# Optimization experiments

Hardware: AMD Instinct MI355X
Metric: run time of the kernel (lower is better)

Reference implementation:

```python
import jax, jax.numpy as jnp
import numpy as np

BS = 16   # block_size
SR = 16   # search_range


def setup_inputs() -> dict:
    key = jax.random.key(0)
    k1, k2 = jax.random.split(key)
    H, W = 2048, 2048
    current_frame = jax.random.uniform(k1, (H, W), dtype=jnp.float32)
    reference_frame = jax.random.uniform(k2, (H, W), dtype=jnp.float32)
    return {"current_frame": current_frame, "reference_frame": reference_frame}


def reference(current_frame, reference_frame):
    H, W = current_frame.shape
    bs, sr = BS, SR
    nby, nbx = H // bs, W // bs
    # zero-pad reference by search_range on all sides (matches F.pad constant 0)
    ref_p = jnp.pad(reference_frame, sr)
    # offsets in the same iteration order as the torch loops: dy outer, dx inner
    d = jnp.arange(-sr, sr + 1, dtype=jnp.int32)
    offs = jnp.stack(jnp.meshgrid(d, d, indexing="ij"), axis=-1).reshape(-1, 2)  # [(2sr+1)^2, 2]

    init = (
        jnp.full((nby, nbx), jnp.inf, dtype=jnp.float32),   # min_sad
        jnp.zeros((nby, nbx), dtype=jnp.float32),            # motion_x
        jnp.zeros((nby, nbx), dtype=jnp.float32),            # motion_y
    )

    def step(carry, off):
        best_sad, mx, my = carry
        dy, dx = off[0], off[1]
        # shifted reference plane: ref_padded[sr+dy : sr+dy+H, sr+dx : sr+dx+W]
        ref_shift = jax.lax.dynamic_slice(ref_p, (sr + dy, sr + dx), (H, W))
        # per-block SAD: sum |cur - ref| over each bs x bs tile
        sad = jnp.abs(current_frame - ref_shift).reshape(nby, bs, nbx, bs).sum(axis=(1, 3))
        better = sad < best_sad
        new_carry = (
            jnp.where(better, sad, best_sad),
            jnp.where(better, dx.astype(jnp.float32), mx),
            jnp.where(better, dy.astype(jnp.float32), my),
        )
        return new_carry, None

    (min_sad, motion_x, motion_y), _ = jax.lax.scan(step, init, offs)
    return motion_x, motion_y, min_sad
```

## Files before the change

### kernel.cpp

```cpp
#include <hip/hip_runtime.h>


#define HH 2048
#define WW 2048
#define NB 128
#define RSTR 100
#define CSTR 64
#define SCALE 16777216.0f
#define INV_SCALE 5.9604644775390625e-08f

__device__ __forceinline__ unsigned sadacc(unsigned a, unsigned b, unsigned c) {
    unsigned d;
    asm("v_sad_u32 %0, %1, %2, %3" : "=v"(d) : "v"(a), "v"(b), "v"(c));
    return d;
}

__launch_bounds__(256, 2)
__global__ void me_kernel(const float* __restrict__ cur,
                          const float* __restrict__ ref,
                          float* __restrict__ out) {
    __shared__ __align__(16) unsigned lds_ref[48 * RSTR];
    __shared__ __align__(16) unsigned lds_cur[16 * CSTR];

    const int tid = threadIdx.x;
    const int wg  = blockIdx.x;
    const int by  = wg >> 5;
    const int bx0 = (wg & 31) << 2;

    const int gy0 = by * 16 - 16;
    const int gx0 = bx0 * 16 - 16;
    for (int i = tid; i < 48 * 96; i += 256) {
        int r = i / 96;
        int c = i - r * 96;
        int gy = gy0 + r, gx = gx0 + c;
        float v = 0.f;
        if (gy >= 0 && gy < HH && gx >= 0 && gx < WW) v = ref[gy * WW + gx];
        lds_ref[r * RSTR + c] = (unsigned)(v * SCALE);
    }
    for (int i = tid; i < 16 * 64; i += 256) {
        int r = i >> 6, c = i & 63;
        lds_cur[i] = (unsigned)(cur[(by * 16 + r) * WW + bx0 * 16 + c] * SCALE);
    }
    __syncthreads();

    const int l  = tid & 63;
    const int b  = tid >> 6;
    const int n  = l >> 1;
    const int m  = l & 1;
    const int cb = b * 16;

    unsigned acc[16];
#pragma unroll
    for (int d = 0; d < 16; ++d) acc[d] = 0u;
    unsigned eA = 0u, eB = 0u;

    const unsigned* refbase = &lds_ref[n * RSTR + cb + 16 * m];
    const unsigned* curbase = &lds_cur[cb];
    const unsigned* eAbase  = &lds_ref[32 * RSTR + cb];
    const unsigned* eBbase  = &lds_ref[l * RSTR + cb + 32];

#pragma unroll 4
    for (int y = 0; y < 16; ++y) {
        unsigned cu[16];
#pragma unroll
        for (int q = 0; q < 4; ++q) {
            uint4 v = *(const uint4*)&curbase[y * CSTR + 4 * q];
            cu[4*q+0] = v.x; cu[4*q+1] = v.y; cu[4*q+2] = v.z; cu[4*q+3] = v.w;
        }
        unsigned rf[32];
#pragma unroll
        for (int q = 0; q < 8; ++q) {
            uint4 v = *(const uint4*)&refbase[y * RSTR + 4 * q];
            rf[4*q+0] = v.x; rf[4*q+1] = v.y; rf[4*q+2] = v.z; rf[4*q+3] = v.w;
        }
#pragma unroll
        for (int dd = 0; dd < 16; ++dd)
#pragma unroll
            for (int x = 0; x < 16; ++x)
                acc[dd] = sadacc(cu[x], rf[dd + x], acc[dd]);

        if (l < 33) {
#pragma unroll
            for (int x = 0; x < 16; ++x)
                eA = sadacc(cu[x], eAbase[y * RSTR + l + x], eA);
            unsigned eb[16];
#pragma unroll
            for (int q = 0; q < 4; ++q) {
                uint4 v = *(const uint4*)&eBbase[y * RSTR + 4 * q];
                eb[4*q+0] = v.x; eb[4*q+1] = v.y; eb[4*q+2] = v.z; eb[4*q+3] = v.w;
            }
#pragma unroll
            for (int x = 0; x < 16; ++x)
                eB = sadacc(cu[x], eb[x], eB);
        }
    }

    unsigned long long best = ~0ull;
#pragma unroll
    for (int dd = 0; dd < 16; ++dd) {
        unsigned long long p =
            ((unsigned long long)acc[dd] << 32) | (unsigned)(n * 33 + 16 * m + dd);
        best = p < best ? p : best;
    }
    if (l < 33) {
        unsigned long long pA =
            ((unsigned long long)eA << 32) | (unsigned)(32 * 33 + l);
        best = pA < best ? pA : best;
        unsigned long long pB =
            ((unsigned long long)eB << 32) | (unsigned)(l * 33 + 32);
        best = pB < best ? pB : best;
    }
#pragma unroll
    for (int s = 32; s > 0; s >>= 1) {
        unsigned long long o = __shfl_xor(best, s, 64);
        best = o < best ? o : best;
    }
    if (l == 0) {
        unsigned idx = (unsigned)(best & 0xffffffffu);
        unsigned sadu = (unsigned)(best >> 32);
        int dy = (int)(idx / 33) - 16;
        int dx = (int)(idx % 33) - 16;
        int bi = by * NB + (bx0 + b);
        out[bi]             = (float)dx;
        out[16384 + bi]     = (float)dy;
        out[2 * 16384 + bi] = (float)sadu * INV_SCALE;
    }
}

extern "C" void kernel_launch(void* const* d_in, const int* in_sizes, int n_in,
                              void* d_out, int out_size, void* d_ws, size_t ws_size,
                              hipStream_t stream) {
    const float* cur = (const float*)d_in[0];
    const float* ref = (const float*)d_in[1];
    float* out = (float*)d_out;
    (void)in_sizes; (void)n_in; (void)out_size; (void)d_ws; (void)ws_size;
    me_kernel<<<dim3(4096), dim3(256), 0, stream>>>(cur, ref, out);
}
```

Before: 219.4 us.

## Widen workgroup to eight blocks and rebalance edge-offset SAD work

Each workgroup now covers eight horizontally adjacent 16x16 blocks with 512 threads, sharing a 48x160 reference window. This cuts the halo loaded per block compared with four blocks per group. The two divergent edge-SAD paths, taken only by lanes below 33, become a single edge SAD per lane across all 64 lanes. The last corner offset is computed cooperatively with a wave reduction. The launch bounds change to (512, 8), which caps registers per thread and may cause spills given the 16 accumulators, 32 reference values and 16 current values held per thread.

Result: faster. 211.7 us (-3.5%).

```diff
diff --git a/kernel.cpp b/kernel.cpp
--- a/kernel.cpp
+++ b/kernel.cpp
@@ -4,18 +4,16 @@
 #define HH 2048
 #define WW 2048
 #define NB 128
-#define RSTR 100
-#define CSTR 64
+#define RSTR 164
+#define CSTR 128
 #define SCALE 16777216.0f
 #define INV_SCALE 5.9604644775390625e-08f
 
-__device__ __forceinline__ unsigned sadacc(unsigned a, unsigned b, unsigned c) {
-    unsigned d;
-    asm("v_sad_u32 %0, %1, %2, %3" : "=v"(d) : "v"(a), "v"(b), "v"(c));
-    return d;
+__device__ __forceinline__ void sadacc(unsigned a, unsigned b, unsigned& c) {
+    asm("v_sad_u32 %0, %1, %2, %0" : "+v"(c) : "v"(a), "v"(b));
 }
 
-__launch_bounds__(256, 2)
+__launch_bounds__(512, 8)
 __global__ void me_kernel(const float* __restrict__ cur,
                           const float* __restrict__ ref,
                           float* __restrict__ out) {
@@ -24,21 +22,25 @@
 
     const int tid = threadIdx.x;
     const int wg  = blockIdx.x;
-    const int by  = wg >> 5;
-    const int bx0 = (wg & 31) << 2;
+    const int by  = wg >> 4;
+    const int bx0 = (wg & 15) << 3;
 
     const int gy0 = by * 16 - 16;
     const int gx0 = bx0 * 16 - 16;
-    for (int i = tid; i < 48 * 96; i += 256) {
-        int r = i / 96;
-        int c = i - r * 96;
+#pragma unroll
+    for (int k = 0; k < 15; ++k) {
+        int i = tid + k * 512;
+        int r = i / 160;
+        int c = i - r * 160;
         int gy = gy0 + r, gx = gx0 + c;
         float v = 0.f;
         if (gy >= 0 && gy < HH && gx >= 0 && gx < WW) v = ref[gy * WW + gx];
         lds_ref[r * RSTR + c] = (unsigned)(v * SCALE);
     }
-    for (int i = tid; i < 16 * 64; i += 256) {
-        int r = i >> 6, c = i & 63;
+#pragma unroll
+    for (int k = 0; k < 4; ++k) {
+        int i = tid + k * 512;
+        int r = i >> 7, c = i & 127;
         lds_cur[i] = (unsigned)(cur[(by * 16 + r) * WW + bx0 * 16 + c] * SCALE);
     }
     __syncthreads();
@@ -52,12 +54,12 @@
     unsigned acc[16];
 #pragma unroll
     for (int d = 0; d < 16; ++d) acc[d] = 0u;
-    unsigned eA = 0u, eB = 0u;
+    unsigned eacc = 0u;
 
     const unsigned* refbase = &lds_ref[n * RSTR + cb + 16 * m];
     const unsigned* curbase = &lds_cur[cb];
-    const unsigned* eAbase  = &lds_ref[32 * RSTR + cb];
-    const unsigned* eBbase  = &lds_ref[l * RSTR + cb + 32];
+    const unsigned* ebase = (l < 33) ? &lds_ref[32 * RSTR + cb + l]
+                                     : &lds_ref[(l - 33) * RSTR + cb + 32];
 
 #pragma unroll 4
     for (int y = 0; y < 16; ++y) {
@@ -77,22 +79,10 @@
         for (int dd = 0; dd < 16; ++dd)
 #pragma unroll
             for (int x = 0; x < 16; ++x)
-                acc[dd] = sadacc(cu[x], rf[dd + x], acc[dd]);
-
-        if (l < 33) {
+                sadacc(cu[x], rf[dd + x], acc[dd]);
 #pragma unroll
-            for (int x = 0; x < 16; ++x)
-                eA = sadacc(cu[x], eAbase[y * RSTR + l + x], eA);
-            unsigned eb[16];
-#pragma unroll
-            for (int q = 0; q < 4; ++q) {
-                uint4 v = *(const uint4*)&eBbase[y * RSTR + 4 * q];
-                eb[4*q+0] = v.x; eb[4*q+1] = v.y; eb[4*q+2] = v.z; eb[4*q+3] = v.w;
-            }
-#pragma unroll
-            for (int x = 0; x < 16; ++x)
-                eB = sadacc(cu[x], eb[x], eB);
-        }
+        for (int x = 0; x < 16; ++x)
+            sadacc(cu[x], ebase[y * RSTR + x], eacc);
     }
 
     unsigned long long best = ~0ull;
@@ -102,21 +92,30 @@
             ((unsigned long long)acc[dd] << 32) | (unsigned)(n * 33 + 16 * m + dd);
         best = p < best ? p : best;
     }
-    if (l < 33) {
-        unsigned long long pA =
-            ((unsigned long long)eA << 32) | (unsigned)(32 * 33 + l);
-        best = pA < best ? pA : best;
-        unsigned long long pB =
-            ((unsigned long long)eB << 32) | (unsigned)(l * 33 + 32);
-        best = pB < best ? pB : best;
+    {
+        unsigned eidx = (l < 33) ? (unsigned)(32 * 33 + l) : (unsigned)((l - 33) * 33 + 32);
+        unsigned long long p = ((unsigned long long)eacc << 32) | eidx;
+        best = p < best ? p : best;
+    }
+    {
+        int r = l >> 2, c0 = (l & 3) * 4;
+        unsigned s = 0u;
+        uint4 cv = *(const uint4*)&lds_cur[r * CSTR + cb + c0];
+        uint4 rv = *(const uint4*)&lds_ref[(31 + r) * RSTR + cb + 32 + c0];
+        sadacc(cv.x, rv.x, s); sadacc(cv.y, rv.y, s);
+        sadacc(cv.z, rv.z, s); sadacc(cv.w, rv.w, s);
+#pragma unroll
+        for (int sh = 32; sh > 0; sh >>= 1) s += __shfl_xor(s, sh, 64);
+        unsigned long long p = ((unsigned long long)s << 32) | 1055u;
+        best = p < best ? p : best;
     }
 #pragma unroll
-    for (int s = 32; s > 0; s >>= 1) {
-        unsigned long long o = __shfl_xor(best, s, 64);
+    for (int sh = 32; sh > 0; sh >>= 1) {
+        unsigned long long o = __shfl_xor(best, sh, 64);
         best = o < best ? o : best;
     }
     if (l == 0) {
-        unsigned idx = (unsigned)(best & 0xffffffffu);
+        unsigned idx  = (unsigned)(best & 0xffffffffu);
         unsigned sadu = (unsigned)(best >> 32);
         int dy = (int)(idx / 33) - 16;
         int dx = (int)(idx % 33) - 16;
@@ -134,5 +133,5 @@
     const float* ref = (const float*)d_in[1];
     float* out = (float*)d_out;
     (void)in_sizes; (void)n_in; (void)out_size; (void)d_ws; (void)ws_size;
-    me_kernel<<<dim3(4096), dim3(256), 0, stream>>>(cur, ref, out);
+    me_kernel<<<dim3(2048), dim3(512), 0, stream>>>(cur, ref, out);
 }
```
